# Kernel optimization log

Measured on AMD Instinct MI355X. Metric: run time of the kernel, lower is better.

The kernel has to match this reference:

```python
import jax, jax.numpy as jnp
import numpy as np
from math import comb

# ---- static config (mirrors BezierLossConfig / module init) ----
N_DEG = 8          # polynomial degree (= self.degree, len of coefficient vector)
D_BEZ = 7          # bezier_degree d
M_SAMPLES = 131072 # cfg.samples_per_segment
DISC_EPS = 1e-12
LEAD_EPS = 1e-12
DELTA_SOFT = 1e-6
EPS_SOFT = 1e-12
ALPHA = 0.1
BETA = 0.01


def setup_inputs() -> dict:
    key = jax.random.key(0)
    k0, k1, k2 = jax.random.split(key, 3)
    P0 = jax.random.normal(k0, (N_DEG, 2), dtype=jnp.float32)
    Pd = jax.random.normal(k1, (N_DEG, 2), dtype=jnp.float32)
    P_mid = jax.random.normal(k2, (D_BEZ - 1, N_DEG, 2), dtype=jnp.float32)
    ts = jnp.linspace(0.0, 1.0, M_SAMPLES, dtype=jnp.float32)  # make_uniform_ts
    return {"P0": P0, "Pd": Pd, "P_mid": P_mid, "ts": ts}


def _bezier_eval(P_ctrl, ts):
    """Explicit Bernstein evaluation. P_ctrl: (d+1, n, 2), ts: (M,) -> (M, n, 2)."""
    d = P_ctrl.shape[0] - 1
    k = jnp.arange(d + 1, dtype=ts.dtype)
    binom = jnp.asarray([comb(d, i) for i in range(d + 1)], dtype=ts.dtype)
    t = ts[:, None]
    B = binom * jnp.power(t, k) * jnp.power(1.0 - t, d - k)  # (M, d+1)
    return jnp.einsum('mk,knc->mnc', B, P_ctrl)


def _deriv_ctrl(P_ctrl):
    """Derivative control points: Q_k = d * (P_{k+1} - P_k)."""
    d = P_ctrl.shape[0] - 1
    return d * (P_ctrl[1:] - P_ctrl[:-1])


def _complex_norm(X):
    """X: (M, n, 2) -> (M,) complex-vector 2-norm."""
    return jnp.sqrt(jnp.sum(X * X, axis=(1, 2)))


def _disc_logabs(T):
    """log|disc| of monic poly x^n + sum_i T_i x^{n-1-i} via Sylvester resultant.
    T: (M, n, 2) real/imag coefficient samples."""
    M = T.shape[0]
    n = N_DEG
    pc = (T[..., 0] + 1j * T[..., 1]).astype(jnp.complex64)        # (M, n)
    f = jnp.concatenate([jnp.ones((M, 1), jnp.complex64), pc], 1)  # (M, n+1) descending
    dk = (n - jnp.arange(n)).astype(jnp.complex64)                 # n, n-1, ..., 1
    g = f[:, :n] * dk                                              # (M, n) f' descending
    s = 2 * n - 1
    S = jnp.zeros((M, s, s), jnp.complex64)
    for i in range(n - 1):          # n-1 shifted rows of f (small fixed loop)
        S = S.at[:, i, i:i + n + 1].set(f)
    for j in range(n):              # n shifted rows of g
        S = S.at[:, n - 1 + j, j:j + n].set(g)
    _, logabsdet = jnp.linalg.slogdet(S)                           # (M,) real
    log_eps = jnp.log(jnp.asarray(DISC_EPS, logabsdet.dtype))
    # disc = Res(f,f') / lead, lead = 1 (monic)
    return jnp.logaddexp(logabsdet, log_eps) - jnp.log(jnp.asarray(1.0 + LEAD_EPS, logabsdet.dtype))


def reference(P0, Pd, P_mid, ts):
    P_ctrl = jnp.concatenate([P0[None], P_mid, Pd[None]], axis=0)  # (d+1, n, 2)
    T = _bezier_eval(P_ctrl, ts)                                   # (M, n, 2)
    Q_ctrl = _deriv_ctrl(P_ctrl)
    Tp = _bezier_eval(Q_ctrl, ts)
    speed = _complex_norm(Tp)                                      # (M,)

    disc_logabs = _disc_logabs(T)                                  # (M,)
    # softabs in log domain: log sqrt(exp(2L) + delta^2)
    log_delta2 = 2.0 * jnp.log(jnp.asarray(DELTA_SOFT, disc_logabs.dtype))
    log_softabs = 0.5 * jnp.logaddexp(2.0 * disc_logabs, log_delta2)
    log_softabs_eps = jnp.logaddexp(log_softabs, jnp.log(jnp.asarray(EPS_SOFT, disc_logabs.dtype)))
    w = jnp.exp(-(log_softabs_eps / float(N_DEG)).astype(speed.dtype))

    L_cl = jnp.mean(speed * w)
    L_d1 = jnp.sqrt(jnp.mean(speed * speed))
    R_ctrl = _deriv_ctrl(Q_ctrl)
    Tpp = _bezier_eval(R_ctrl, ts)
    accel = _complex_norm(Tpp)
    L_d2 = jnp.sqrt(jnp.mean(accel * accel))
    loss = L_cl + ALPHA * L_d1 + BETA * L_d2
    return loss
```

## Files before the change

### kernel.cpp

```cpp
#include <hip/hip_runtime.h>
#include <math.h>

#define M_SAMPLES 131072
#define NBLK 512
#define BLK 256

__device__ __forceinline__ float logaddexp_f(float a, float b) {
    float m = fmaxf(a, b);
    float d = fminf(a, b) - m;
    return m + __logf(1.f + __expf(d));
}

__device__ const float BINOM[8][8] = {
  {1,0,0,0,0,0,0,0},{1,1,0,0,0,0,0,0},{1,2,1,0,0,0,0,0},{1,3,3,1,0,0,0,0},
  {1,4,6,4,1,0,0,0},{1,5,10,10,5,1,0,0},{1,6,15,20,15,6,1,0},{1,7,21,35,35,21,7,1}};

__global__ __launch_bounds__(BLK) void bez_main_kernel(
    const float* __restrict__ P0, const float* __restrict__ Pd,
    const float* __restrict__ Pmid, const float* __restrict__ ts,
    float* __restrict__ partial)
{
    __shared__ float sP[8][8][2];
    __shared__ float sA[8][8][2];
    __shared__ float red[4][3];

    const int tid = threadIdx.x;
    if (tid < 16) { sP[0][tid >> 1][tid & 1] = P0[tid]; sP[7][tid >> 1][tid & 1] = Pd[tid]; }
    if (tid < 96) { int r = tid / 16, rem = tid % 16; sP[1 + r][rem >> 1][rem & 1] = Pmid[tid]; }
    __syncthreads();
    if (tid < 128) {
        int m = tid >> 4, rem = tid & 15, j = rem >> 1, c = rem & 1;
        float acc = 0.f;
        float sgn = (m & 1) ? -1.f : 1.f;
        for (int k = 0; k <= m; ++k) {
            acc += sgn * BINOM[m][k] * sP[k][j][c];
            sgn = -sgn;
        }
        sA[m][j][c] = BINOM[7][m] * acc;
    }
    __syncthreads();

    const int gid = blockIdx.x * BLK + tid;
    const float t = ts[gid];

    float Tr[8], Ti[8];
    float sp2 = 0.f, ac2 = 0.f;
#pragma unroll
    for (int j = 0; j < 8; ++j) {
        float pr = sA[7][j][0], pi = sA[7][j][1];
        float qr = 0.f, qi = 0.f;
        float rr = 0.f, ri = 0.f;
#pragma unroll
        for (int m = 6; m >= 0; --m) {
            rr = rr * t + qr; ri = ri * t + qi;
            qr = qr * t + pr; qi = qi * t + pi;
            pr = pr * t + sA[m][j][0]; pi = pi * t + sA[m][j][1];
        }
        Tr[j] = pr; Ti[j] = pi;
        sp2 += qr * qr + qi * qi;
        ac2 += rr * rr + ri * ri;
    }
    ac2 *= 4.f;
    const float speed = sqrtf(sp2);

    float fr[9], fi[9];
#pragma unroll
    for (int j = 0; j < 8; ++j) { fr[j] = Tr[7 - j]; fi[j] = Ti[7 - j]; }
    fr[8] = 1.f; fi[8] = 0.f;
    float ur[9], uii[9];
#pragma unroll
    for (int k = 1; k < 9; ++k) { ur[k] = (float)k * fr[k]; uii[k] = (float)k * fi[k]; }

    float cR[8][8], cI[8][8];
#pragma unroll
    for (int a = 0; a < 8; ++a) {
#pragma unroll
        for (int b = a + 1; b < 8; ++b) {
            cR[a][b] = (fr[a] * ur[b + 1] - fi[a] * uii[b + 1]) - (fr[b] * ur[a + 1] - fi[b] * uii[a + 1]);
            cI[a][b] = (fr[a] * uii[b + 1] + fi[a] * ur[b + 1]) - (fr[b] * uii[a + 1] + fi[b] * ur[a + 1]);
        }
    }

    float Br[8][8], Bi[8][8];
#pragma unroll
    for (int j = 0; j < 8; ++j) { Br[7][j] = ur[j + 1]; Bi[7][j] = uii[j + 1]; }
#pragma unroll
    for (int i = 7; i >= 1; --i) {
#pragma unroll
        for (int j = 0; j < 8; ++j) {
            float cr, ci;
            if (i < j)      { cr = cR[i][j];  ci = cI[i][j]; }
            else if (i > j) { cr = -cR[j][i]; ci = -cI[j][i]; }
            else            { cr = 0.f;       ci = 0.f; }
            if (j >= 1) { cr += Br[i][j - 1]; ci += Bi[i][j - 1]; }
            Br[i - 1][j] = cr; Bi[i - 1][j] = ci;
        }
    }

    float logm = 1.f; int loge = 0;
#pragma unroll
    for (int k = 0; k < 8; ++k) {
        float dr = Br[k][k], di = Bi[k][k];
        float pm2 = dr * dr + di * di;
        unsigned ub = __float_as_uint(pm2);
        loge += (int)(ub >> 23) - 126;
        logm *= __uint_as_float((ub & 0x007fffffu) | 0x3f000000u);
        if (k < 7) {
            float is = __builtin_amdgcn_rcpf(pm2);
            is = (pm2 > 1e-30f) ? is : 0.f;
            float ivr = dr * is, ivi = -di * is;
            float wr[8], wi[8];
#pragma unroll
            for (int i = k + 1; i < 8; ++i) {
                float ar = Br[k][i], ai = Bi[k][i];
                wr[i] = ar * ivr - ai * ivi;
                wi[i] = ar * ivi + ai * ivr;
            }
#pragma unroll
            for (int i = k + 1; i < 8; ++i) {
#pragma unroll
                for (int j = i; j < 8; ++j) {
                    float br = Br[k][j], bi2 = Bi[k][j];
                    Br[i][j] -= wr[i] * br - wi[i] * bi2;
                    Bi[i][j] -= wr[i] * bi2 + wi[i] * br;
                }
            }
        }
    }
    float logdet = 0.5f * (__logf(logm) + (float)loge * 0.69314718055994531f);

    const float LOG_DISC_EPS = -27.63102111592855f;
    const float LOG_DELTA2  = -27.63102111592855f;
    const float LOG1P_LEAD  = 1e-12f;
    float disc_logabs = logaddexp_f(logdet, LOG_DISC_EPS) - LOG1P_LEAD;
    float log_softabs = 0.5f * logaddexp_f(2.f * disc_logabs, LOG_DELTA2);
    float log_softabs_eps = logaddexp_f(log_softabs, LOG_DISC_EPS);
    float w = __expf(-log_softabs_eps * 0.125f);

    float v1 = speed * w, v2 = sp2, v3 = ac2;
#pragma unroll
    for (int off = 32; off; off >>= 1) {
        v1 += __shfl_down(v1, off);
        v2 += __shfl_down(v2, off);
        v3 += __shfl_down(v3, off);
    }
    const int wid = tid >> 6, lane = tid & 63;
    if (lane == 0) { red[wid][0] = v1; red[wid][1] = v2; red[wid][2] = v3; }
    __syncthreads();
    if (tid == 0) {
        float s1 = 0.f, s2 = 0.f, s3 = 0.f;
        for (int w2 = 0; w2 < 4; ++w2) { s1 += red[w2][0]; s2 += red[w2][1]; s3 += red[w2][2]; }
        partial[blockIdx.x * 3 + 0] = s1;
        partial[blockIdx.x * 3 + 1] = s2;
        partial[blockIdx.x * 3 + 2] = s3;
    }
}

__global__ __launch_bounds__(NBLK) void bez_finalize_kernel(
    const float* __restrict__ partial, float* __restrict__ out)
{
    const int tid = threadIdx.x;
    float v1 = partial[tid * 3 + 0];
    float v2 = partial[tid * 3 + 1];
    float v3 = partial[tid * 3 + 2];
#pragma unroll
    for (int off = 32; off; off >>= 1) {
        v1 += __shfl_down(v1, off);
        v2 += __shfl_down(v2, off);
        v3 += __shfl_down(v3, off);
    }
    __shared__ float red[8][3];
    const int wid = tid >> 6, lane = tid & 63;
    if (lane == 0) { red[wid][0] = v1; red[wid][1] = v2; red[wid][2] = v3; }
    __syncthreads();
    if (tid == 0) {
        float s1 = 0.f, s2 = 0.f, s3 = 0.f;
        for (int w2 = 0; w2 < 8; ++w2) { s1 += red[w2][0]; s2 += red[w2][1]; s3 += red[w2][2]; }
        const float Mf = (float)M_SAMPLES;
        out[0] = s1 / Mf + 0.1f * sqrtf(s2 / Mf) + 0.01f * sqrtf(s3 / Mf);
    }
}

extern "C" void kernel_launch(void* const* d_in, const int* in_sizes, int n_in,
                              void* d_out, int out_size, void* d_ws, size_t ws_size,
                              hipStream_t stream) {
    const float* P0   = (const float*)d_in[0];
    const float* Pd   = (const float*)d_in[1];
    const float* Pmid = (const float*)d_in[2];
    const float* ts   = (const float*)d_in[3];
    float* out = (float*)d_out;
    float* partial = (float*)d_ws;

    bez_main_kernel<<<NBLK, BLK, 0, stream>>>(P0, Pd, Pmid, ts, partial);
    bez_finalize_kernel<<<1, NBLK, 0, stream>>>(partial, out);
}
```

Before: 15.00 us.

## Precompute squared-speed polynomials and shrink blocks to single wavefronts

Per block, computes the coefficients of |T'(t)|^2 and |T''(t)|^2 as scalar polynomials in t. Each thread then evaluates these with short Horner chains instead of carrying derivative Horner recurrences for all 8 complex coefficients. Blocks shrink to 64 threads (one wavefront) with 2048 blocks, which removes the shared-memory cross-wave reduction, and the finalize kernel loops over more partials. The cofactor terms are computed inside the elimination loop to shorten their live ranges, and the ts load is hoisted ahead of setup. Risks: more blocks each repeating the coefficient setup, and a little rounding error from the expanded polynomials, clamped at zero.

```diff
diff --git a/kernel.cpp b/kernel.cpp
--- a/kernel.cpp
+++ b/kernel.cpp
@@ -2,8 +2,9 @@
 #include <math.h>
 
 #define M_SAMPLES 131072
-#define NBLK 512
-#define BLK 256
+#define BLK 64
+#define NBLK (M_SAMPLES / BLK)
+#define BLKF 256
 
 __device__ __forceinline__ float logaddexp_f(float a, float b) {
     float m = fmaxf(a, b);
@@ -15,83 +16,110 @@
   {1,0,0,0,0,0,0,0},{1,1,0,0,0,0,0,0},{1,2,1,0,0,0,0,0},{1,3,3,1,0,0,0,0},
   {1,4,6,4,1,0,0,0},{1,5,10,10,5,1,0,0},{1,6,15,20,15,6,1,0},{1,7,21,35,35,21,7,1}};
 
-__global__ __launch_bounds__(BLK) void bez_main_kernel(
+__global__ __launch_bounds__(BLK, 2) void bez_main_kernel(
     const float* __restrict__ P0, const float* __restrict__ Pd,
     const float* __restrict__ Pmid, const float* __restrict__ ts,
     float* __restrict__ partial)
 {
     __shared__ float sP[8][8][2];
-    __shared__ float sA[8][8][2];
-    __shared__ float red[4][3];
+    __shared__ float2 sA2[8][8];
+    __shared__ float sSP2[13];
+    __shared__ float sAC2[11];
 
     const int tid = threadIdx.x;
+    const int gid = blockIdx.x * BLK + tid;
+    const float t = ts[gid];
+
     if (tid < 16) { sP[0][tid >> 1][tid & 1] = P0[tid]; sP[7][tid >> 1][tid & 1] = Pd[tid]; }
-    if (tid < 96) { int r = tid / 16, rem = tid % 16; sP[1 + r][rem >> 1][rem & 1] = Pmid[tid]; }
-    __syncthreads();
-    if (tid < 128) {
-        int m = tid >> 4, rem = tid & 15, j = rem >> 1, c = rem & 1;
-        float acc = 0.f;
+    for (int e = tid; e < 96; e += BLK) {
+        int r = e / 16, rem = e % 16;
+        sP[1 + r][rem >> 1][rem & 1] = Pmid[e];
+    }
+    __syncthreads();
+    {
+        int m = tid >> 3, j = tid & 7;
+        float aR = 0.f, aI = 0.f;
         float sgn = (m & 1) ? -1.f : 1.f;
         for (int k = 0; k <= m; ++k) {
-            acc += sgn * BINOM[m][k] * sP[k][j][c];
+            aR += sgn * BINOM[m][k] * sP[k][j][0];
+            aI += sgn * BINOM[m][k] * sP[k][j][1];
             sgn = -sgn;
         }
-        sA[m][j][c] = BINOM[7][m] * acc;
-    }
-    __syncthreads();
-
-    const int gid = blockIdx.x * BLK + tid;
-    const float t = ts[gid];
-
-    float Tr[8], Ti[8];
-    float sp2 = 0.f, ac2 = 0.f;
+        sA2[m][j] = make_float2(BINOM[7][m] * aR, BINOM[7][m] * aI);
+    }
+    __syncthreads();
+    if (tid < 13) {
+        int d = tid; float s = 0.f;
+        int lo = d > 6 ? d - 6 : 0, hi = d < 6 ? d : 6;
+        for (int m = lo; m <= hi; ++m) {
+            int mp = d - m;
+            float wgt = (float)((m + 1) * (mp + 1));
+            for (int j = 0; j < 8; ++j) {
+                float2 a = sA2[m + 1][j], b = sA2[mp + 1][j];
+                s += wgt * (a.x * b.x + a.y * b.y);
+            }
+        }
+        sSP2[d] = s;
+    } else if (tid < 24) {
+        int d = tid - 13; float s = 0.f;
+        int lo = d > 5 ? d - 5 : 0, hi = d < 5 ? d : 5;
+        for (int m = lo; m <= hi; ++m) {
+            int mp = d - m;
+            float wgt = (float)((m + 2) * (m + 1) * (mp + 2) * (mp + 1));
+            for (int j = 0; j < 8; ++j) {
+                float2 a = sA2[m + 2][j], b = sA2[mp + 2][j];
+                s += wgt * (a.x * b.x + a.y * b.y);
+            }
+        }
+        sAC2[d] = s;
+    }
+    __syncthreads();
+
+    float fr[9], fi[9];
 #pragma unroll
     for (int j = 0; j < 8; ++j) {
-        float pr = sA[7][j][0], pi = sA[7][j][1];
-        float qr = 0.f, qi = 0.f;
-        float rr = 0.f, ri = 0.f;
+        float2 a7 = sA2[7][j];
+        float pr = a7.x, pi = a7.y;
 #pragma unroll
         for (int m = 6; m >= 0; --m) {
-            rr = rr * t + qr; ri = ri * t + qi;
-            qr = qr * t + pr; qi = qi * t + pi;
-            pr = pr * t + sA[m][j][0]; pi = pi * t + sA[m][j][1];
-        }
-        Tr[j] = pr; Ti[j] = pi;
-        sp2 += qr * qr + qi * qi;
-        ac2 += rr * rr + ri * ri;
-    }
-    ac2 *= 4.f;
+            float2 a = sA2[m][j];
+            pr = pr * t + a.x; pi = pi * t + a.y;
+        }
+        fr[7 - j] = pr; fi[7 - j] = pi;
+    }
+    fr[8] = 1.f; fi[8] = 0.f;
+
+    float sp2 = sSP2[12];
+#pragma unroll
+    for (int d = 11; d >= 0; --d) sp2 = sp2 * t + sSP2[d];
+    sp2 = fmaxf(sp2, 0.f);
+    float ac2 = sAC2[10];
+#pragma unroll
+    for (int d = 9; d >= 0; --d) ac2 = ac2 * t + sAC2[d];
+    ac2 = fmaxf(ac2, 0.f);
     const float speed = sqrtf(sp2);
 
-    float fr[9], fi[9];
-#pragma unroll
-    for (int j = 0; j < 8; ++j) { fr[j] = Tr[7 - j]; fi[j] = Ti[7 - j]; }
-    fr[8] = 1.f; fi[8] = 0.f;
     float ur[9], uii[9];
 #pragma unroll
     for (int k = 1; k < 9; ++k) { ur[k] = (float)k * fr[k]; uii[k] = (float)k * fi[k]; }
 
-    float cR[8][8], cI[8][8];
-#pragma unroll
-    for (int a = 0; a < 8; ++a) {
-#pragma unroll
-        for (int b = a + 1; b < 8; ++b) {
-            cR[a][b] = (fr[a] * ur[b + 1] - fi[a] * uii[b + 1]) - (fr[b] * ur[a + 1] - fi[b] * uii[a + 1]);
-            cI[a][b] = (fr[a] * uii[b + 1] + fi[a] * ur[b + 1]) - (fr[b] * uii[a + 1] + fi[b] * ur[a + 1]);
-        }
-    }
-
     float Br[8][8], Bi[8][8];
+    float cRr[8][8], cIi[8][8];
 #pragma unroll
     for (int j = 0; j < 8; ++j) { Br[7][j] = ur[j + 1]; Bi[7][j] = uii[j + 1]; }
 #pragma unroll
     for (int i = 7; i >= 1; --i) {
+#pragma unroll
+        for (int j = 0; j < i; ++j) {
+            cRr[j][i] = (fr[j] * ur[i + 1] - fi[j] * uii[i + 1]) - (fr[i] * ur[j + 1] - fi[i] * uii[j + 1]);
+            cIi[j][i] = (fr[j] * uii[i + 1] + fi[j] * ur[i + 1]) - (fr[i] * uii[j + 1] + fi[i] * ur[j + 1]);
+        }
 #pragma unroll
         for (int j = 0; j < 8; ++j) {
             float cr, ci;
-            if (i < j)      { cr = cR[i][j];  ci = cI[i][j]; }
-            else if (i > j) { cr = -cR[j][i]; ci = -cI[j][i]; }
-            else            { cr = 0.f;       ci = 0.f; }
+            if (i < j)      { cr = cRr[i][j];  ci = cIi[i][j]; }
+            else if (i > j) { cr = -cRr[j][i]; ci = -cIi[j][i]; }
+            else            { cr = 0.f;        ci = 0.f; }
             if (j >= 1) { cr += Br[i][j - 1]; ci += Bi[i][j - 1]; }
             Br[i - 1][j] = cr; Bi[i - 1][j] = ci;
         }
@@ -144,38 +172,38 @@
         v2 += __shfl_down(v2, off);
         v3 += __shfl_down(v3, off);
     }
-    const int wid = tid >> 6, lane = tid & 63;
-    if (lane == 0) { red[wid][0] = v1; red[wid][1] = v2; red[wid][2] = v3; }
-    __syncthreads();
     if (tid == 0) {
-        float s1 = 0.f, s2 = 0.f, s3 = 0.f;
-        for (int w2 = 0; w2 < 4; ++w2) { s1 += red[w2][0]; s2 += red[w2][1]; s3 += red[w2][2]; }
-        partial[blockIdx.x * 3 + 0] = s1;
-        partial[blockIdx.x * 3 + 1] = s2;
-        partial[blockIdx.x * 3 + 2] = s3;
-    }
-}
-
-__global__ __launch_bounds__(NBLK) void bez_finalize_kernel(
+        partial[blockIdx.x * 3 + 0] = v1;
+        partial[blockIdx.x * 3 + 1] = v2;
+        partial[blockIdx.x * 3 + 2] = v3;
+    }
+}
+
+__global__ __launch_bounds__(BLKF) void bez_finalize_kernel(
     const float* __restrict__ partial, float* __restrict__ out)
 {
     const int tid = threadIdx.x;
-    float v1 = partial[tid * 3 + 0];
-    float v2 = partial[tid * 3 + 1];
-    float v3 = partial[tid * 3 + 2];
+    float v1 = 0.f, v2 = 0.f, v3 = 0.f;
+#pragma unroll
+    for (int k = 0; k < NBLK / BLKF; ++k) {
+        const int b = tid + k * BLKF;
+        v1 += partial[b * 3 + 0];
+        v2 += partial[b * 3 + 1];
+        v3 += partial[b * 3 + 2];
+    }
 #pragma unroll
     for (int off = 32; off; off >>= 1) {
         v1 += __shfl_down(v1, off);
         v2 += __shfl_down(v2, off);
         v3 += __shfl_down(v3, off);
     }
-    __shared__ float red[8][3];
+    __shared__ float red[4][3];
     const int wid = tid >> 6, lane = tid & 63;
     if (lane == 0) { red[wid][0] = v1; red[wid][1] = v2; red[wid][2] = v3; }
     __syncthreads();
     if (tid == 0) {
         float s1 = 0.f, s2 = 0.f, s3 = 0.f;
-        for (int w2 = 0; w2 < 8; ++w2) { s1 += red[w2][0]; s2 += red[w2][1]; s3 += red[w2][2]; }
+        for (int w2 = 0; w2 < 4; ++w2) { s1 += red[w2][0]; s2 += red[w2][1]; s3 += red[w2][2]; }
         const float Mf = (float)M_SAMPLES;
         out[0] = s1 / Mf + 0.1f * sqrtf(s2 / Mf) + 0.01f * sqrtf(s3 / Mf);
     }
@@ -192,5 +220,5 @@
     float* partial = (float*)d_ws;
 
     bez_main_kernel<<<NBLK, BLK, 0, stream>>>(P0, Pd, Pmid, ts, partial);
-    bez_finalize_kernel<<<1, NBLK, 0, stream>>>(partial, out);
-}
+    bez_finalize_kernel<<<1, BLKF, 0, stream>>>(partial, out);
+}
```

Result: slower. 16.83 us (+12.2%).
